# Kernel optimization log

Measured on AMD Instinct MI355X. Metric: run time of the kernel, lower is better.

## Reference

```python
import jax, jax.numpy as jnp
import numpy as np

B, N, M, U, L = 2048, 256, 128, 512, 2   # batch, memory locations, memory width, num_units, num_layers
RH, WH, SH = 2, 2, 1                      # read heads, write heads, conv_shift_range
CLIP = 20.0
HEAD_R = M + 3 + (2 * SH + 1)             # 134 = k(M)+beta+g+s(2r+1)+gamma
HEAD_W = HEAD_R + 2 * M                   # 390 = + erase(M) + add(M)


def setup_inputs():
    key = jax.random.key(0)
    ks = jax.random.split(key, 12)
    def nrm(k, shape, s=0.05):
        return jax.random.normal(k, shape, jnp.float32) * s
    return {
        "X": jax.random.normal(ks[0], (B, U), jnp.float32),
        "m0": nrm(ks[1], (1, N, M), 0.5),
        "H0": nrm(ks[2], (L, 1, U)),
        "C0": nrm(ks[3], (L, 1, U)),
        "R0": nrm(ks[4], (RH, 1, M)),
        "A0": nrm(ks[5], (RH + WH, 1, N)),
        "W_prep": nrm(ks[6], (M * RH, U)),
        "b_prep": jnp.zeros((U,), jnp.float32),
        "W_lstm": nrm(ks[7], (L, 3 * U, 4 * U)),
        "b_lstm": jnp.zeros((L, 4 * U), jnp.float32),
        "W_r": nrm(ks[8], (U, RH * HEAD_R)),
        "b_r": jnp.zeros((RH * HEAD_R,), jnp.float32),
        "W_w": nrm(ks[9], (U, WH * HEAD_W)),
        "b_w": jnp.zeros((WH * HEAD_W,), jnp.float32),
        "W_ou": nrm(ks[10], (U + RH * M, U)),
        "b_ou": jnp.zeros((U,), jnp.float32),
    }


def _addressing(k, beta, g, s, gamma, m, a_prev):
    # k [B,M], beta/g/gamma [B], s [B,2*SH+1], m [B,N,M], a_prev [B,N]
    inner = jnp.einsum('bnm,bm->bn', m, k)
    k_norm = jnp.sqrt(jnp.sum(k * k, axis=1, keepdims=True))   # [B,1]
    m_norm = jnp.sqrt(jnp.sum(m * m, axis=2))                  # [B,N]
    K = inner / (k_norm * m_norm + 1e-8)
    w_c = jax.nn.softmax(beta[:, None] * K, axis=1)            # exp/sum in source == softmax
    w_g = g[:, None] * w_c + (1.0 - g[:, None]) * a_prev
    # The stacked-slice s_matrix in the source is exactly circular convolution:
    # w_conv[i] = sum_d s_d * w_g[(i - d) mod N], d in {0..SH, -SH..-1} matching s layout.
    shifts = list(range(0, SH + 1)) + list(range(-SH, 0))
    w_conv = sum(s[:, j:j + 1] * jnp.roll(w_g, shifts[j], axis=1) for j in range(2 * SH + 1))
    w_sharp = w_conv ** gamma[:, None]
    return w_sharp / jnp.sum(w_sharp, axis=1, keepdims=True)


def reference(X, m0, H0, C0, R0, A0, W_prep, b_prep, W_lstm, b_lstm,
              W_r, b_r, W_w, b_w, W_ou, b_ou):
    b = X.shape[0]
    m = jnp.broadcast_to(m0, (b, N, M))
    R_prev = [jnp.broadcast_to(jnp.tanh(R0[i]), (b, M)) for i in range(RH)]
    A_prev = [jnp.broadcast_to(jax.nn.softmax(A0[i], axis=-1), (b, N)) for i in range(RH + WH)]

    # controller
    h = jnp.concatenate(R_prev, axis=1) @ W_prep + b_prep
    for l in range(L):
        x_in = jnp.concatenate([X, h], axis=1)                              # [B,2U]
        h_prev = jnp.broadcast_to(H0[l], (b, U))
        c_prev = jnp.broadcast_to(C0[l], (b, U))
        z = jnp.concatenate([x_in, h_prev], axis=1) @ W_lstm[l] + b_lstm[l]  # [B,4U]
        i_g, f_g, g_g, o_g = jnp.split(z, 4, axis=1)
        c = jax.nn.sigmoid(f_g) * c_prev + jax.nn.sigmoid(i_g) * jnp.tanh(g_g)
        h = jax.nn.sigmoid(o_g) * jnp.tanh(c)
    h = jnp.clip(h, -CLIP, CLIP)

    r_heads = (h @ W_r + b_r).reshape(b, RH, HEAD_R)
    w_heads = (h @ W_w + b_w).reshape(b, WH, HEAD_W)
    heads = [r_heads[:, i] for i in range(RH)] + [w_heads[:, i] for i in range(WH)]

    A_t = []
    for ii, hd in enumerate(heads):
        A_t.append(_addressing(
            k=jnp.tanh(hd[:, :M]),
            beta=jax.nn.softplus(hd[:, M]),
            g=jax.nn.sigmoid(hd[:, M + 1]),
            s=jax.nn.softmax(hd[:, M + 2:M + 2 + 2 * SH + 1], axis=-1),
            gamma=jax.nn.softplus(hd[:, M + 2 + 2 * SH + 1]),
            m=m, a_prev=A_prev[ii]))

    # reads from old memory
    R_t = [jnp.einsum('bn,bnm->bm', A_t[i], m) for i in range(RH)]

    # sequential erase/add writes
    m_t = m
    for ii in range(WH):
        w = A_t[RH + ii][:, :, None]                                  # [B,N,1]
        del_v = jax.nn.sigmoid(w_heads[:, ii, -2 * M:-M])[:, None, :]  # [B,1,M]
        add_v = jnp.tanh(w_heads[:, ii, -M:])[:, None, :]
        m_t = m_t * (1.0 - w * del_v) + w * add_v

    y = jnp.clip(jnp.concatenate([h] + R_t, axis=1) @ W_ou + b_ou, -CLIP, CLIP)
    return y, m_t
```

## Files before the change

kernel.cpp:

```cpp
#include <hip/hip_runtime.h>
#include <math.h>

static constexpr int Bn = 2048;
static constexpr int Nn = 256;
static constexpr int Mn = 128;
static constexpr int Un = 512;

static constexpr size_t OFF_MNORM = 4608;
static constexpr size_t OFF_APREV = 4864;
static constexpr size_t OFF_BIASH = 5888;
static constexpr size_t OFF_KMAT  = 16384;
static constexpr size_t OFF_HEADS = OFF_KMAT + (size_t)8192 * 256;
static constexpr size_t OFF_AT    = OFF_HEADS + (size_t)2048 * 1048;
static constexpr size_t OFF_ERA   = OFF_AT + (size_t)2 * 2048 * 256;
static constexpr size_t OFF_ADD   = OFF_ERA + (size_t)2048 * 256;
static constexpr size_t OFF_XHB   = OFF_ADD + (size_t)2048 * 256;
static constexpr size_t OFF_HCAT  = OFF_XHB + 524288;
static constexpr size_t OFF_W0T   = OFF_HCAT + 524288;
static constexpr size_t OFF_W1T   = OFF_W0T + 524288;
static constexpr size_t OFF_WRWT  = OFF_W1T + 1048576;
static constexpr size_t OFF_WCOMB = OFF_WRWT + 294912;
static constexpr size_t OFF_WR2T  = OFF_WCOMB + 262144;
static constexpr size_t OFF_M0B   = OFF_WR2T + 65536;
static constexpr size_t OFF_ZPART = OFF_M0B + 16384 + 524288;

static constexpr int P_X0  = 0;
static constexpr int P_M0  = 512;
static constexpr int P_W0  = 528;
static constexpr int P_WR2 = 1552;
static constexpr int P_CA  = 1680;
static constexpr int P_ZC  = 1681;
static constexpr int P_END = 1745;

static constexpr int M_L0  = 0;
static constexpr int M_PF  = 512;
static constexpr int M_W1  = 544;
static constexpr int M_WRr = 2592;
static constexpr int M_WRw = 2736;
static constexpr int M_WOU = 3136;
static constexpr int M_ZC1 = 3392;
static constexpr int M_END = 3456;

static constexpr int T_OUT = 0;
static constexpr int T_MEM = 128;
static constexpr int T_END = 384;

#define DEV __device__ __forceinline__

typedef __attribute__((ext_vector_type(8))) short bf16x8;
typedef __attribute__((ext_vector_type(4))) float f32x4;
typedef __attribute__((ext_vector_type(8))) unsigned short ushort8;
typedef unsigned int u32;

DEV float sigf(float x) { return 1.0f / (1.0f + expf(-x)); }
DEV float softplusf(float x) { return x > 20.0f ? x : log1pf(expf(x)); }
DEV unsigned short f2bf(float f) {
    unsigned u = __float_as_uint(f);
    u = (u + 0x7FFFu + ((u >> 16) & 1u)) >> 16;
    return (unsigned short)u;
}
DEV void gload16(const unsigned short* g, unsigned short* l) {
    __builtin_amdgcn_global_load_lds(
        (const __attribute__((address_space(1))) u32*)g,
        (__attribute__((address_space(3))) u32*)l, 16, 0, 0);
}

DEV float blk_reduce_max(float v, float* red) {
    int tid = threadIdx.x;
    red[tid] = v; __syncthreads();
    for (int s = (int)blockDim.x >> 1; s > 0; s >>= 1) {
        if (tid < s) red[tid] = fmaxf(red[tid], red[tid + s]);
        __syncthreads();
    }
    float r = red[0]; __syncthreads();
    return r;
}
DEV float blk_reduce_sum(float v, float* red) {
    int tid = threadIdx.x;
    red[tid] = v; __syncthreads();
    for (int s = (int)blockDim.x >> 1; s > 0; s >>= 1) {
        if (tid < s) red[tid] += red[tid + s];
        __syncthreads();
    }
    float r = red[0]; __syncthreads();
    return r;
}

DEV float wv_sum(float v) {
    #pragma unroll
    for (int off = 32; off; off >>= 1) v += __shfl_xor(v, off);
    return v;
}
DEV float wv_max(float v) {
    #pragma unroll
    for (int off = 32; off; off >>= 1) v = fmaxf(v, __shfl_xor(v, off));
    return v;
}
DEV float blk_sum4(float v, float* red4) {
    v = wv_sum(v);
    int w = threadIdx.x >> 6;
    if ((threadIdx.x & 63) == 0) red4[w] = v;
    __syncthreads();
    float r = red4[0] + red4[1] + red4[2] + red4[3];
    __syncthreads();
    return r;
}
DEV float blk_max4(float v, float* red4) {
    v = wv_max(v);
    int w = threadIdx.x >> 6;
    if ((threadIdx.x & 63) == 0) red4[w] = v;
    __syncthreads();
    float r = fmaxf(fmaxf(red4[0], red4[1]), fmaxf(red4[2], red4[3]));
    __syncthreads();
    return r;
}

#define GEMM_SHARED                                                             \
    __shared__ __align__(16) unsigned short As[2][64 * 64];                     \
    __shared__ __align__(16) unsigned short Ws[2][128 * 64];

#define GEMM_REGS                                                               \
    const int tid  = threadIdx.x;                                               \
    const int lane = tid & 63;                                                  \
    const int wave = tid >> 6;                                                  \
    const int wr = wave >> 1, wc = wave & 1;                                    \
    const int ke = ((tid & 7) * 8) ^ (((tid >> 3) & 7) << 3);                   \
    const int frow = lane & 15;                                                 \
    const int fko  = (lane >> 4) * 8;                                           \
    const int fxm  = (frow & 7) << 3;                                           \
    f32x4 acc[2][4];                                                            \
    _Pragma("unroll")                                                           \
    for (int i = 0; i < 2; ++i)                                                 \
        _Pragma("unroll")                                                       \
        for (int j = 0; j < 4; ++j) acc[i][j] = (f32x4){0.f, 0.f, 0.f, 0.f};

#define GEMM_STAGE(buf, k0)                                                     \
    {                                                                           \
        _Pragma("unroll")                                                       \
        for (int q = 0; q < 2; ++q)                                             \
            gload16(A  + (size_t)(row0 + q * 32 + (tid >> 3)) * lda + (k0) + ke,\
                    &As[buf][q * 2048 + tid * 8]);                              \
        _Pragma("unroll")                                                       \
        for (int q = 0; q < 4; ++q)                                             \
            gload16(Wt + (size_t)(col0 + q * 32 + (tid >> 3)) * ldw + (k0) + ke,\
                    &Ws[buf][q * 2048 + tid * 8]);                              \
    }

#define GEMM_FRAGS_AND_MFMA(Ab, Wb)                                             \
    {                                                                           \
        bf16x8 af[2][2], wf[2][4];                                              \
        _Pragma("unroll")                                                       \
        for (int kk = 0; kk < 2; ++kk) {                                        \
            _Pragma("unroll")                                                   \
            for (int i = 0; i < 2; ++i) {                                       \
                int fr = wr * 32 + i * 16 + frow;                               \
                af[kk][i] = *(const bf16x8*)&(Ab)[fr * 64 + ((kk * 32 + fko) ^ fxm)]; \
            }                                                                   \
            _Pragma("unroll")                                                   \
            for (int j = 0; j < 4; ++j) {                                       \
                int fr = wc * 64 + j * 16 + frow;                               \
                wf[kk][j] = *(const bf16x8*)&(Wb)[fr * 64 + ((kk * 32 + fko) ^ fxm)]; \
            }                                                                   \
        }                                                                       \
        __builtin_amdgcn_s_setprio(1);                                          \
        _Pragma("unroll")                                                       \
        for (int kk = 0; kk < 2; ++kk)                                          \
            _Pragma("unroll")                                                   \
            for (int i = 0; i < 2; ++i)                                         \
                _Pragma("unroll")                                               \
                for (int j = 0; j < 4; ++j)                                     \
                    acc[i][j] = __builtin_amdgcn_mfma_f32_16x16x32_bf16(        \
                        af[kk][i], wf[kk][j], acc[i][j], 0, 0, 0);              \
        __builtin_amdgcn_s_setprio(0);                                          \
    }

#define GEMM_MAINLOOP(Kr)                                                       \
    {                                                                           \
        const int nt = (Kr) >> 6;                                               \
        int cur = 0;                                                            \
        GEMM_STAGE(0, 0);                                                       \
        for (int t = 0; t < nt; ++t) {                                          \
            if (t + 1 < nt) {                                                   \
                GEMM_STAGE(cur ^ 1, (t + 1) * 64);                              \
                asm volatile("s_waitcnt vmcnt(6)" ::: "memory");                \
            } else {                                                            \
                asm volatile("s_waitcnt vmcnt(0)" ::: "memory");                \
            }                                                                   \
            __builtin_amdgcn_sched_barrier(0);                                  \
            __builtin_amdgcn_s_barrier();                                       \
            __builtin_amdgcn_sched_barrier(0);                                  \
            GEMM_FRAGS_AND_MFMA(As[cur], Ws[cur]);                              \
            __builtin_amdgcn_sched_barrier(0);                                  \
            __builtin_amdgcn_s_barrier();                                       \
            cur ^= 1;                                                           \
        }                                                                       \
    }

#define LSTM_EPILOGUE(zc, doclip, houtp, ldhv)                                  \
    {                                                                           \
        const int uu = lane & 15;                                               \
        const int q  = (col0 >> 6) + wc;                                        \
        const int uq = q * 16 + uu;                                             \
        const float c0v = c0[(zc) * 512 + uq];                                  \
        float bg[4];                                                            \
        _Pragma("unroll")                                                       \
        for (int g = 0; g < 4; ++g) {                                           \
            int j = g * 512 + q * 16 + uu;                                      \
            float a = b_lstm[(zc) * 2048 + j];                                  \
            _Pragma("unroll")                                                   \
            for (int p = 0; p < 8; ++p)                                         \
                a += zpart[((size_t)(zc) * 8 + p) * 2048 + j];                  \
            bg[g] = a;                                                          \
        }                                                                       \
        _Pragma("unroll")                                                       \
        for (int i = 0; i < 2; ++i) {                                           \
            int rbase = row0 + wr * 32 + i * 16 + (lane >> 4) * 4;              \
            _Pragma("unroll")                                                   \
            for (int r = 0; r < 4; ++r) {                                       \
                float ig = acc[i][0][r] + bg[0];                                \
                float fg = acc[i][1][r] + bg[1];                                \
                float gg = acc[i][2][r] + bg[2];                                \
                float og = acc[i][3][r] + bg[3];                                \
                float c = sigf(fg) * c0v + sigf(ig) * tanhf(gg);                \
                float h = sigf(og) * tanhf(c);                                  \
                if (doclip) h = fminf(fmaxf(h, -20.f), 20.f);                   \
                (houtp)[(size_t)(rbase + r) * (ldhv) + uq] = f2bf(h);           \
            }                                                                   \
        }                                                                       \
    }

DEV void dev_cvt8(const float* src, int lds, unsigned short* dst, int ldd,
                  int c8, int bloc, int tid)
{
    size_t idx = (size_t)bloc * 256 + tid;
    size_t r = idx / c8, c = (idx % c8) * 8;
    const float* s = src + r * lds + c;
    float4 v0 = *(const float4*)s;
    float4 v1 = *(const float4*)(s + 4);
    ushort8 o;
    o[0] = f2bf(v0.x); o[1] = f2bf(v0.y); o[2] = f2bf(v0.z); o[3] = f2bf(v0.w);
    o[4] = f2bf(v1.x); o[5] = f2bf(v1.y); o[6] = f2bf(v1.z); o[7] = f2bf(v1.w);
    *(ushort8*)(dst + r * ldd + c) = o;
}

DEV void dev_cvtT(const float* src, int R, int C, int lds,
                  unsigned short* dst, int ldd, int mode, int bx, int by,
                  int tid, float* t )
{
    const int x = tid & 31;
    for (int y = tid >> 5; y < 32; y += 8) {
        int r = by * 32 + y, c = bx * 32 + x;
        int scol = c;
        if (mode) scol = ((c >> 4) & 3) * 512 + (c >> 6) * 16 + (c & 15);
        t[y * 33 + x] = (r < R && c < C) ? src[(size_t)r * lds + scol] : 0.f;
    }
    __syncthreads();
    for (int y = tid >> 5; y < 32; y += 8) {
        int c = bx * 32 + y, r = by * 32 + x;
        if (c < C && r < R) dst[(size_t)c * ldd + r] = f2bf(t[x * 33 + y]);
    }
}

__global__ __launch_bounds__(256) void k_prep(
    const float* __restrict__ X, const float* __restrict__ m0,
    const float* __restrict__ H0, const float* __restrict__ R0,
    const float* __restrict__ A0, const float* __restrict__ W_prep,
    const float* __restrict__ b_prep, const float* __restrict__ W_lstm,
    const float* __restrict__ b_r, const float* __restrict__ b_w,
    const float* __restrict__ W_ou, float* __restrict__ ws)
{
    __shared__ float sh[32 * 33 + 64];
    const int bid = blockIdx.x, tid = threadIdx.x;
    unsigned short* XHB  = (unsigned short*)(ws + OFF_XHB);
    unsigned short* W0T  = (unsigned short*)(ws + OFF_W0T);
    unsigned short* WR2T = (unsigned short*)(ws + OFF_WR2T);
    unsigned short* M0B  = (unsigned short*)(ws + OFF_M0B);

    if (bid < P_M0) {
        dev_cvt8(X, 512, XHB, 1024, 64, bid - P_X0, tid);
    } else if (bid < P_W0) {
        dev_cvt8(m0, 128, M0B, 128, 16, bid - P_M0, tid);
    } else if (bid < P_WR2) {
        int s = bid - P_W0;
        dev_cvtT(W_lstm, 512, 2048, 2048, W0T, 512, 1, s & 63, s >> 6, tid, sh);
    } else if (bid < P_CA) {
        int s = bid - P_WR2;
        dev_cvtT(W_ou + (size_t)512 * 512, 256, 512, 512, WR2T, 256, 0,
                 s & 15, s >> 4, tid, sh);
    } else if (bid < P_ZC) {
        float* red = sh;
        for (int i = 0; i < 4; ++i) {
            float v = A0[i * 256 + tid];
            float mx = blk_reduce_max(v, red);
            float e = expf(v - mx);
            float s = blk_reduce_sum(e, red);
            ws[OFF_APREV + i * 256 + tid] = e / s;
        }
        float acc = 0.f;
        for (int m = 0; m < 128; ++m) {
            float t = m0[(size_t)tid * 128 + m];
            acc = fmaf(t, t, acc);
        }
        ws[OFF_MNORM + tid] = sqrtf(acc);
        for (int j = tid; j < 1152; j += 256)
            ws[OFF_BIASH + j] = (j < 268) ? b_r[j] : (j < 1048 ? b_w[j - 268] : 0.f);
    } else {
        int sub = bid - P_ZC;
        int colb = sub & 7, up = sub >> 3;
        int j = colb * 256 + tid;
        float acc = 0.f;
        if (up < 4) {
            sh[256 + tid] = tanhf(R0[tid]);
            __syncthreads();
            if (tid < 128) {
                int u = up * 128 + tid;
                float a = b_prep[u];
                for (int k = 0; k < 256; ++k)
                    a = fmaf(sh[256 + k], W_prep[(size_t)k * 512 + u], a);
                sh[tid] = a;
            }
            __syncthreads();
            const int u0 = up * 128;
            #pragma unroll 4
            for (int t = 0; t < 128; ++t)
                acc = fmaf(sh[t], W_lstm[(size_t)(512 + u0 + t) * 2048 + j], acc);
        } else {
            const int u0 = up * 128;
            #pragma unroll 4
            for (int t = 0; t < 128; ++t)
                acc = fmaf(H0[u0 - 512 + t],
                           W_lstm[(size_t)(512 + u0 + t) * 2048 + j], acc);
        }
        (ws + OFF_ZPART)[(size_t)up * 2048 + j] = acc;
    }
}

__global__ __launch_bounds__(256) void k_mid(
    const float* __restrict__ W_lstm, const float* __restrict__ W_r,
    const float* __restrict__ W_w, const float* __restrict__ W_ou,
    const float* __restrict__ H0, const float* __restrict__ b_lstm,
    const float* __restrict__ c0, float* __restrict__ ws)
{
    GEMM_SHARED
    const int s = blockIdx.x;
    float* sh = (float*)&As[0][0];
    unsigned short* XHB   = (unsigned short*)(ws + OFF_XHB);
    unsigned short* W0T   = (unsigned short*)(ws + OFF_W0T);
    unsigned short* W1T   = (unsigned short*)(ws + OFF_W1T);
    unsigned short* WRWT  = (unsigned short*)(ws + OFF_WRWT);
    unsigned short* WCOMB = (unsigned short*)(ws + OFF_WCOMB);
    unsigned short* WR2T  = (unsigned short*)(ws + OFF_WR2T);
    unsigned short* M0B   = (unsigned short*)(ws + OFF_M0B);
    const float* zpart    = ws + OFF_ZPART;

    if (s < M_W1) {
        const unsigned short *A, *Wt;
        int lda, ldw, row0, col0, Kr;
        unsigned short* pCb = nullptr;
        const bool lstm0 = (s < M_PF);
        if (lstm0) {
            A = XHB;  lda = 1024; Wt = W0T; ldw = 512;
            row0 = (s & 31) * 64; col0 = (s >> 5) * 128; Kr = 512;
        } else {
            int p = s - M_PF;
            int pz = p >> 4, py = (p >> 3) & 1, px = p & 7;
            A = WR2T + pz * 128; lda = 256; Wt = M0B; ldw = 128;
            row0 = px * 64; col0 = py * 128; Kr = 128;
            pCb = WCOMB + 512 + pz * 256;
        }
        GEMM_REGS
        GEMM_MAINLOOP(Kr)
        if (lstm0) {
            unsigned short* hout = XHB + 512;
            LSTM_EPILOGUE(0, 0, hout, 1024)
        } else {
            #pragma unroll
            for (int i = 0; i < 2; ++i) {
                int m0r = row0 + wr * 32 + i * 16 + (lane >> 4) * 4;
                #pragma unroll
                for (int j = 0; j < 4; ++j) {
                    int n = col0 + wc * 64 + j * 16 + (lane & 15);
                    #pragma unroll
                    for (int r = 0; r < 4; ++r)
                        pCb[(size_t)(m0r + r) * 1024 + n] = f2bf(acc[i][j][r]);
                }
            }
        }
    } else if (s < M_WRr) {
        int s1 = s - M_W1;
        dev_cvtT(W_lstm + (size_t)1536 * 2048, 1024, 2048, 2048, W1T, 1024, 1,
                 s1 & 63, s1 >> 6, threadIdx.x, sh);
    } else if (s < M_WRw) {
        int s2 = s - M_WRr;
        dev_cvtT(W_r, 512, 268, 268, WRWT, 512, 0, s2 % 9, s2 / 9, threadIdx.x, sh);
    } else if (s < M_WOU) {
        int s3 = s - M_WRw;
        dev_cvtT(W_w, 512, 780, 780, WRWT + (size_t)268 * 512, 512, 0,
                 s3 % 25, s3 / 25, threadIdx.x, sh);
    } else if (s < M_ZC1) {
        int s4 = s - M_WOU;
        dev_cvtT(W_ou, 512, 512, 512, WCOMB, 1024, 0, s4 & 15, s4 >> 4,
                 threadIdx.x, sh);
    } else {
        int s5 = s - M_ZC1;
        int colb = s5 & 7, up = s5 >> 3;
        int j = colb * 256 + threadIdx.x;
        const int u0 = up * 64;
        const float* W1 = W_lstm + (size_t)1536 * 2048;
        float acc = 0.f;
        #pragma unroll 4
        for (int t = 0; t < 64; ++t)
            acc = fmaf(H0[512 + u0 + t], W1[(size_t)(1024 + u0 + t) * 2048 + j], acc);
        (ws + OFF_ZPART)[((size_t)8 + up) * 2048 + j] = acc;
    }
}

__global__ __launch_bounds__(256) void gemm_lstm(
    const unsigned short* __restrict__ A, int lda,
    const unsigned short* __restrict__ Wt, int ldw,
    const float* __restrict__ zpart, const float* __restrict__ b_lstm,
    const float* __restrict__ c0, unsigned short* __restrict__ hout)
{
    GEMM_SHARED
    const int row0 = blockIdx.x * 64;
    const int col0 = blockIdx.y * 128;
    GEMM_REGS
    GEMM_MAINLOOP(1024)
    LSTM_EPILOGUE(1, 1, hout, 1024)
}

__global__ __launch_bounds__(256) void gemm_bf16(
    const unsigned short* __restrict__ A, int lda,
    const unsigned short* __restrict__ Wt, int ldw,
    const float* __restrict__ bias, float* __restrict__ C, int ldc,
    int Nr, int Kr)
{
    GEMM_SHARED
    const int row0 = blockIdx.x * 64;
    const int col0 = blockIdx.y * 128;
    GEMM_REGS
    GEMM_MAINLOOP(Kr)
    #pragma unroll
    for (int i = 0; i < 2; ++i) {
        int m0r = row0 + wr * 32 + i * 16 + (lane >> 4) * 4;
        #pragma unroll
        for (int j = 0; j < 4; ++j) {
            int n = col0 + wc * 64 + j * 16 + (lane & 15);
            if (n >= Nr) continue;
            float bv = bias ? bias[n] : 0.f;
            #pragma unroll
            for (int r = 0; r < 4; ++r)
                C[(size_t)(m0r + r) * ldc + n] = acc[i][j][r] + bv;
        }
    }
}

__global__ __launch_bounds__(256) void gemm_kmat(
    const float* __restrict__ heads,
    const unsigned short* __restrict__ M0B,
    float* __restrict__ C)
{
    GEMM_SHARED
    const int row0 = blockIdx.x * 64;
    const int col0 = blockIdx.y * 128;
    GEMM_REGS

#define KMAT_STAGE(buf, k0)                                                     \
    {                                                                           \
        _Pragma("unroll")                                                       \
        for (int q = 0; q < 2; ++q) {                                           \
            int R = row0 + q * 32 + (tid >> 3);                                 \
            int b = R >> 2, ih = R & 3;                                         \
            int cb = (ih < 2) ? ih * 134 : 268 + (ih - 2) * 390;                \
            const float* hp = heads + (size_t)b * 1048 + cb + (k0) + ke;        \
            ushort8 o;                                                          \
            _Pragma("unroll")                                                   \
            for (int j = 0; j < 8; ++j) o[j] = f2bf(tanhf(hp[j]));              \
            *(ushort8*)&As[buf][q * 2048 + tid * 8] = o;                        \
        }                                                                       \
        _Pragma("unroll")                                                       \
        for (int q = 0; q < 4; ++q)                                             \
            gload16(M0B + (size_t)(col0 + q * 32 + (tid >> 3)) * 128 + (k0) + ke,\
                    &Ws[buf][q * 2048 + tid * 8]);                              \
    }

    int cur = 0;
    KMAT_STAGE(0, 0);
    for (int t = 0; t < 2; ++t) {
        __syncthreads();
        if (t == 0) KMAT_STAGE(1, 64);
        GEMM_FRAGS_AND_MFMA(As[cur], Ws[cur]);
        cur ^= 1;
    }
#undef KMAT_STAGE
    #pragma unroll
    for (int i = 0; i < 2; ++i) {
        int m0r = row0 + wr * 32 + i * 16 + (lane >> 4) * 4;
        #pragma unroll
        for (int j = 0; j < 4; ++j) {
            int n = col0 + wc * 64 + j * 16 + (lane & 15);
            #pragma unroll
            for (int r = 0; r < 4; ++r)
                C[(size_t)(m0r + r) * 256 + n] = acc[i][j][r];
        }
    }
}

__global__ __launch_bounds__(256) void k_addr(
    const float* __restrict__ heads, const float* __restrict__ kmat,
    const float* __restrict__ mnorm, const float* __restrict__ aprev,
    float* __restrict__ at, unsigned short* __restrict__ hcat,
    float* __restrict__ era, float* __restrict__ addv)
{
    __shared__ float red4[4];
    __shared__ float wgs[256];
    __shared__ float sc[6];
    const int b = blockIdx.x, i = blockIdx.y, tid = threadIdx.x;
    const int cb = (i < 2) ? i * 134 : 268 + (i - 2) * 390;
    const float* hd = heads + (size_t)b * 1048 + cb;
    float kv = (tid < 128) ? tanhf(hd[tid]) : 0.f;
    float kn = sqrtf(blk_sum4(kv * kv, red4));
    if (i >= 2 && tid < 128) {
        era [((size_t)b * 2 + (i - 2)) * 128 + tid] = sigf(hd[134 + tid]);
        addv[((size_t)b * 2 + (i - 2)) * 128 + tid] = tanhf(hd[262 + tid]);
    }
    if (tid == 0) {
        sc[0] = softplusf(hd[128]);
        sc[1] = sigf(hd[129]);
        float v0 = hd[130], v1 = hd[131], v2 = hd[132];
        float mx = fmaxf(v0, fmaxf(v1, v2));
        float e0 = expf(v0 - mx), e1 = expf(v1 - mx), e2 = expf(v2 - mx);
        float ssum = e0 + e1 + e2;
        sc[2] = e0 / ssum; sc[3] = e1 / ssum; sc[4] = e2 / ssum;
        sc[5] = softplusf(hd[133]);
    }
    __syncthreads();
    const float beta = sc[0], g = sc[1], s0 = sc[2], s1 = sc[3], s2 = sc[4],
                gamma = sc[5];
    float inner = kmat[((size_t)b * 4 + i) * 256 + tid];
    float K = inner / (kn * mnorm[tid] + 1e-8f);
    float x = beta * K;
    float mx = blk_max4(x, red4);
    float e = expf(x - mx);
    float se = blk_sum4(e, red4);
    float wc = e / se;
    float wg = g * wc + (1.f - g) * aprev[i * 256 + tid];
    wgs[tid] = wg;
    __syncthreads();
    float wconv = s0 * wg + s1 * wgs[(tid + 255) & 255] + s2 * wgs[(tid + 1) & 255];
    float wsh = powf(wconv, gamma);
    float ssum = blk_sum4(wsh, red4);
    float w = wsh / ssum;
    if (i < 2) hcat[(size_t)b * 1024 + 512 + i * 256 + tid] = f2bf(w);
    else       at[((size_t)(i - 2) * Bn + b) * 256 + tid] = w;
}

__global__ __launch_bounds__(256) void k_tail(
    const unsigned short* __restrict__ HCAT,
    const unsigned short* __restrict__ WCOMB,
    const float* __restrict__ b_ou,
    const float* __restrict__ m0, const float* __restrict__ at,
    const float* __restrict__ era, const float* __restrict__ addv,
    float* __restrict__ out)
{
    GEMM_SHARED
    const int s = blockIdx.x;
    if (s < T_MEM) {
        const unsigned short* A  = HCAT;  const int lda = 1024;
        const unsigned short* Wt = WCOMB; const int ldw = 1024;
        const int row0 = (s & 31) * 64;
        const int col0 = (s >> 5) * 128;
        GEMM_REGS
        GEMM_MAINLOOP(1024)
        #pragma unroll
        for (int i = 0; i < 2; ++i) {
            int m0r = row0 + wr * 32 + i * 16 + (lane >> 4) * 4;
            #pragma unroll
            for (int j = 0; j < 4; ++j) {
                int n = col0 + wc * 64 + j * 16 + (lane & 15);
                if (n >= 512) continue;
                float bv = b_ou[n];
                #pragma unroll
                for (int r = 0; r < 4; ++r) {
                    float v = acc[i][j][r] + bv;
                    out[(size_t)(m0r + r) * 512 + n] = fminf(fmaxf(v, -20.f), 20.f);
                }
            }
        }
    } else {
        const int tid = threadIdx.x;
        const int b0 = (s - T_MEM) * 8;
        float (*at_s)[8][256] = (float(*)[8][256])(&As[0][0]);
        float (*er_s)[8][128] = (float(*)[8][128])(&Ws[0][0]);
        float (*ad_s)[8][128] = (float(*)[8][128])(&Ws[0][4096]);
        for (int t = tid; t < 1024; t += 256) {
            int i = t >> 9, rem = t & 511;
            int bb = rem >> 6, n4 = rem & 63;
            ((float4*)&at_s[i][bb][0])[n4] =
                ((const float4*)(at + ((size_t)i * Bn + b0 + bb) * 256))[n4];
        }
        for (int t = tid; t < 512; t += 256) {
            int i = t >> 8, rem = t & 255;
            int bb = rem >> 5, m4 = rem & 31;
            ((float4*)&er_s[i][bb][0])[m4] =
                ((const float4*)(era + ((size_t)(b0 + bb) * 2 + i) * 128))[m4];
            ((float4*)&ad_s[i][bb][0])[m4] =
                ((const float4*)(addv + ((size_t)(b0 + bb) * 2 + i) * 128))[m4];
        }
        __syncthreads();
        const float4* m0v = (const float4*)m0;
        float4* outv = (float4*)(out + (size_t)Bn * Un);
        for (int pos = tid; pos < 8192; pos += 256) {
            int mq = pos & 31, n = pos >> 5;
            float4 t0 = m0v[pos];
            #pragma unroll
            for (int bb = 0; bb < 8; ++bb) {
                float w0 = at_s[0][bb][n], w1 = at_s[1][bb][n];
                float4 e0 = *(const float4*)&er_s[0][bb][mq * 4];
                float4 a0 = *(const float4*)&ad_s[0][bb][mq * 4];
                float4 e1 = *(const float4*)&er_s[1][bb][mq * 4];
                float4 a1 = *(const float4*)&ad_s[1][bb][mq * 4];
                float4 t = t0;
#define UPD(c) { t.c = t.c * (1.f - w0 * e0.c) + w0 * a0.c; \
                 t.c = t.c * (1.f - w1 * e1.c) + w1 * a1.c; }
                UPD(x) UPD(y) UPD(z) UPD(w)
#undef UPD
                __builtin_nontemporal_store(*(f32x4*)&t,
                    (f32x4*)&outv[(size_t)(b0 + bb) * 8192 + pos]);
            }
        }
    }
}

extern "C" void kernel_launch(void* const* d_in, const int* in_sizes, int n_in,
                              void* d_out, int out_size, void* d_ws, size_t ws_size,
                              hipStream_t stream)
{
    const float* X      = (const float*)d_in[0];
    const float* m0     = (const float*)d_in[1];
    const float* H0     = (const float*)d_in[2];
    const float* C0     = (const float*)d_in[3];
    const float* R0     = (const float*)d_in[4];
    const float* A0     = (const float*)d_in[5];
    const float* W_prep = (const float*)d_in[6];
    const float* b_prep = (const float*)d_in[7];
    const float* W_lstm = (const float*)d_in[8];
    const float* b_lstm = (const float*)d_in[9];
    const float* W_r    = (const float*)d_in[10];
    const float* b_r    = (const float*)d_in[11];
    const float* W_w    = (const float*)d_in[12];
    const float* b_w    = (const float*)d_in[13];
    const float* W_ou   = (const float*)d_in[14];
    const float* b_ou   = (const float*)d_in[15];
    float* ws  = (float*)d_ws;
    float* out = (float*)d_out;

    unsigned short* XHB   = (unsigned short*)(ws + OFF_XHB);
    unsigned short* HCAT  = (unsigned short*)(ws + OFF_HCAT);
    unsigned short* W1T   = (unsigned short*)(ws + OFF_W1T);
    unsigned short* WRWT  = (unsigned short*)(ws + OFF_WRWT);
    unsigned short* WCOMB = (unsigned short*)(ws + OFF_WCOMB);
    unsigned short* M0B   = (unsigned short*)(ws + OFF_M0B);

    k_prep<<<P_END, 256, 0, stream>>>(
        X, m0, H0, R0, A0, W_prep, b_prep, W_lstm, b_r, b_w, W_ou, ws);

    k_mid<<<M_END, 256, 0, stream>>>(
        W_lstm, W_r, W_w, W_ou, H0, b_lstm, C0, ws);

    gemm_lstm<<<dim3(32, 16), 256, 0, stream>>>(
        XHB, 1024, W1T, 1024, ws + OFF_ZPART, b_lstm, C0, HCAT);

    gemm_bf16<<<dim3(32, 9), 256, 0, stream>>>(
        HCAT, 1024, WRWT, 512, ws + OFF_BIASH, ws + OFF_HEADS, 1048, 1048, 512);

    gemm_kmat<<<dim3(128, 2), 256, 0, stream>>>(
        ws + OFF_HEADS, M0B, ws + OFF_KMAT);

    k_addr<<<dim3(Bn, 4), 256, 0, stream>>>(
        ws + OFF_HEADS, ws + OFF_KMAT, ws + OFF_MNORM, ws + OFF_APREV,
        ws + OFF_AT, HCAT, ws + OFF_ERA, ws + OFF_ADD);

    k_tail<<<T_END, 256, 0, stream>>>(
        HCAT, WCOMB, b_ou, m0, ws + OFF_AT, ws + OFF_ERA, ws + OFF_ADD, out);
}
```

Before: 175.7 us.

## Split LSTM layer-1 and output GEMMs to move independent halves earlier

The layer-1 LSTM GEMM is split. The X-dependent half (x times W1 input rows) is now computed in k_mid alongside layer 0 and stored as bf16 in the KMAT scratch region, so gemm_lstm runs only K=512 over the h0 half and adds the stored partial in its epilogue. Likewise, the h-part of the output projection is computed in the new k_heads kernel next to the head GEMM, which leaves k_tail with only the read-vector half. The W1 transpose moves into k_prep. The intent is to shorten the serial critical path and fill more CUs per launch, at the cost of extra bf16/fp32 intermediate traffic and bf16 rounding of the partial sum.

```diff
diff --git a/kernel.cpp b/kernel.cpp
--- a/kernel.cpp
+++ b/kernel.cpp
@@ -10,36 +10,42 @@
 static constexpr size_t OFF_APREV = 4864;
 static constexpr size_t OFF_BIASH = 5888;
 static constexpr size_t OFF_KMAT  = 16384;
-static constexpr size_t OFF_HEADS = OFF_KMAT + (size_t)8192 * 256;
-static constexpr size_t OFF_AT    = OFF_HEADS + (size_t)2048 * 1048;
-static constexpr size_t OFF_ERA   = OFF_AT + (size_t)2 * 2048 * 256;
-static constexpr size_t OFF_ADD   = OFF_ERA + (size_t)2048 * 256;
-static constexpr size_t OFF_XHB   = OFF_ADD + (size_t)2048 * 256;
-static constexpr size_t OFF_HCAT  = OFF_XHB + 524288;
-static constexpr size_t OFF_W0T   = OFF_HCAT + 524288;
+static constexpr size_t OFF_HEADS = OFF_KMAT + 2097152;
+static constexpr size_t OFF_AT    = OFF_HEADS + 2146304;
+static constexpr size_t OFF_ERA   = OFF_AT + 1048576;
+static constexpr size_t OFF_ADD   = OFF_ERA + 524288;
+static constexpr size_t OFF_XHB   = OFF_ADD + 524288;
+static constexpr size_t OFF_HCAT  = OFF_XHB + 1048576;
+static constexpr size_t OFF_W0T   = OFF_HCAT + 1048576;
 static constexpr size_t OFF_W1T   = OFF_W0T + 524288;
 static constexpr size_t OFF_WRWT  = OFF_W1T + 1048576;
 static constexpr size_t OFF_WCOMB = OFF_WRWT + 294912;
 static constexpr size_t OFF_WR2T  = OFF_WCOMB + 262144;
 static constexpr size_t OFF_M0B   = OFF_WR2T + 65536;
-static constexpr size_t OFF_ZPART = OFF_M0B + 16384 + 524288;
+static constexpr size_t OFF_ZPART = OFF_M0B + 16384;
+static constexpr size_t OFF_YH    = OFF_ZPART + 32768;
 
 static constexpr int P_X0  = 0;
 static constexpr int P_M0  = 512;
 static constexpr int P_W0  = 528;
-static constexpr int P_WR2 = 1552;
-static constexpr int P_CA  = 1680;
-static constexpr int P_ZC  = 1681;
-static constexpr int P_END = 1745;
+static constexpr int P_W1  = 1552;
+static constexpr int P_WR2 = 3600;
+static constexpr int P_CA  = 3728;
+static constexpr int P_ZC  = 3729;
+static constexpr int P_END = 3793;
 
 static constexpr int M_L0  = 0;
-static constexpr int M_PF  = 512;
-static constexpr int M_W1  = 544;
-static constexpr int M_WRr = 2592;
-static constexpr int M_WRw = 2736;
-static constexpr int M_WOU = 3136;
-static constexpr int M_ZC1 = 3392;
-static constexpr int M_END = 3456;
+static constexpr int M_ZX  = 512;
+static constexpr int M_PF  = 1024;
+static constexpr int M_WRr = 1056;
+static constexpr int M_WRw = 1200;
+static constexpr int M_WOU = 1600;
+static constexpr int M_ZC1 = 1856;
+static constexpr int M_END = 1920;
+
+static constexpr int H_HD  = 0;
+static constexpr int H_YH  = 288;
+static constexpr int H_END = 416;
 
 static constexpr int T_OUT = 0;
 static constexpr int T_MEM = 128;
@@ -59,6 +65,7 @@
     u = (u + 0x7FFFu + ((u >> 16) & 1u)) >> 16;
     return (unsigned short)u;
 }
+DEV float b2f(unsigned short u) { return __uint_as_float((u32)u << 16); }
 DEV void gload16(const unsigned short* g, unsigned short* l) {
     __builtin_amdgcn_global_load_lds(
         (const __attribute__((address_space(1))) u32*)g,
@@ -196,7 +203,7 @@
         }                                                                       \
     }
 
-#define LSTM_EPILOGUE(zc, doclip, houtp, ldhv)                                  \
+#define LSTM_EPILOGUE(zc, doclip, houtp, ldhv, ZXP)                             \
     {                                                                           \
         const int uu = lane & 15;                                               \
         const int q  = (col0 >> 6) + wc;                                        \
@@ -217,10 +224,17 @@
             int rbase = row0 + wr * 32 + i * 16 + (lane >> 4) * 4;              \
             _Pragma("unroll")                                                   \
             for (int r = 0; r < 4; ++r) {                                       \
-                float ig = acc[i][0][r] + bg[0];                                \
-                float fg = acc[i][1][r] + bg[1];                                \
-                float gg = acc[i][2][r] + bg[2];                                \
-                float og = acc[i][3][r] + bg[3];                                \
+                float z0 = 0.f, z1 = 0.f, z2 = 0.f, z3 = 0.f;                   \
+                if (ZXP) {                                                      \
+                    const unsigned short* zr = (ZXP) +                          \
+                        (size_t)(rbase + r) * 2048 + q * 64 + uu;               \
+                    z0 = b2f(zr[0]);  z1 = b2f(zr[16]);                         \
+                    z2 = b2f(zr[32]); z3 = b2f(zr[48]);                         \
+                }                                                               \
+                float ig = acc[i][0][r] + bg[0] + z0;                           \
+                float fg = acc[i][1][r] + bg[1] + z1;                           \
+                float gg = acc[i][2][r] + bg[2] + z2;                           \
+                float og = acc[i][3][r] + bg[3] + z3;                           \
                 float c = sigf(fg) * c0v + sigf(ig) * tanhf(gg);                \
                 float h = sigf(og) * tanhf(c);                                  \
                 if (doclip) h = fminf(fmaxf(h, -20.f), 20.f);                   \
@@ -273,6 +287,7 @@
     const int bid = blockIdx.x, tid = threadIdx.x;
     unsigned short* XHB  = (unsigned short*)(ws + OFF_XHB);
     unsigned short* W0T  = (unsigned short*)(ws + OFF_W0T);
+    unsigned short* W1T  = (unsigned short*)(ws + OFF_W1T);
     unsigned short* WR2T = (unsigned short*)(ws + OFF_WR2T);
     unsigned short* M0B  = (unsigned short*)(ws + OFF_M0B);
 
@@ -280,9 +295,13 @@
         dev_cvt8(X, 512, XHB, 1024, 64, bid - P_X0, tid);
     } else if (bid < P_W0) {
         dev_cvt8(m0, 128, M0B, 128, 16, bid - P_M0, tid);
-    } else if (bid < P_WR2) {
+    } else if (bid < P_W1) {
         int s = bid - P_W0;
         dev_cvtT(W_lstm, 512, 2048, 2048, W0T, 512, 1, s & 63, s >> 6, tid, sh);
+    } else if (bid < P_WR2) {
+        int s = bid - P_W1;
+        dev_cvtT(W_lstm + (size_t)1536 * 2048, 1024, 2048, 2048, W1T, 1024, 1,
+                 s & 63, s >> 6, tid, sh);
     } else if (bid < P_CA) {
         int s = bid - P_WR2;
         dev_cvtT(W_ou + (size_t)512 * 512, 256, 512, 512, WR2T, 256, 0,
@@ -351,18 +370,25 @@
     unsigned short* WCOMB = (unsigned short*)(ws + OFF_WCOMB);
     unsigned short* WR2T  = (unsigned short*)(ws + OFF_WR2T);
     unsigned short* M0B   = (unsigned short*)(ws + OFF_M0B);
+    unsigned short* ZX    = (unsigned short*)(ws + OFF_KMAT);
     const float* zpart    = ws + OFF_ZPART;
 
-    if (s < M_W1) {
+    if (s < M_WRr) {
         const unsigned short *A, *Wt;
-        int lda, ldw, row0, col0, Kr;
+        int lda, ldw, row0, col0, Kr, mode;
         unsigned short* pCb = nullptr;
-        const bool lstm0 = (s < M_PF);
-        if (lstm0) {
+        if (s < M_ZX) {
+            mode = 0;
             A = XHB;  lda = 1024; Wt = W0T; ldw = 512;
             row0 = (s & 31) * 64; col0 = (s >> 5) * 128; Kr = 512;
+        } else if (s < M_PF) {
+            int p = s - M_ZX;
+            mode = 1;
+            A = XHB;  lda = 1024; Wt = W1T; ldw = 1024;
+            row0 = (p & 31) * 64; col0 = (p >> 5) * 128; Kr = 512;
         } else {
             int p = s - M_PF;
+            mode = 2;
             int pz = p >> 4, py = (p >> 3) & 1, px = p & 7;
             A = WR2T + pz * 128; lda = 256; Wt = M0B; ldw = 128;
             row0 = px * 64; col0 = py * 128; Kr = 128;
@@ -370,9 +396,22 @@
         }
         GEMM_REGS
         GEMM_MAINLOOP(Kr)
-        if (lstm0) {
+        if (mode == 0) {
             unsigned short* hout = XHB + 512;
-            LSTM_EPILOGUE(0, 0, hout, 1024)
+            const unsigned short* zxn = nullptr;
+            LSTM_EPILOGUE(0, 0, hout, 1024, zxn)
+        } else if (mode == 1) {
+            #pragma unroll
+            for (int i = 0; i < 2; ++i) {
+                int m0r = row0 + wr * 32 + i * 16 + (lane >> 4) * 4;
+                #pragma unroll
+                for (int j = 0; j < 4; ++j) {
+                    int n = col0 + wc * 64 + j * 16 + (lane & 15);
+                    #pragma unroll
+                    for (int r = 0; r < 4; ++r)
+                        ZX[(size_t)(m0r + r) * 2048 + n] = f2bf(acc[i][j][r]);
+                }
+            }
         } else {
             #pragma unroll
             for (int i = 0; i < 2; ++i) {
@@ -386,10 +425,6 @@
                 }
             }
         }
-    } else if (s < M_WRr) {
-        int s1 = s - M_W1;
-        dev_cvtT(W_lstm + (size_t)1536 * 2048, 1024, 2048, 2048, W1T, 1024, 1,
-                 s1 & 63, s1 >> 6, threadIdx.x, sh);
     } else if (s < M_WRw) {
         int s2 = s - M_WRr;
         dev_cvtT(W_r, 512, 268, 268, WRWT, 512, 0, s2 % 9, s2 / 9, threadIdx.x, sh);
@@ -419,38 +454,64 @@
     const unsigned short* __restrict__ A, int lda,
     const unsigned short* __restrict__ Wt, int ldw,
     const float* __restrict__ zpart, const float* __restrict__ b_lstm,
-    const float* __restrict__ c0, unsigned short* __restrict__ hout)
+    const float* __restrict__ c0, const unsigned short* __restrict__ ZXP,
+    unsigned short* __restrict__ hout)
 {
     GEMM_SHARED
     const int row0 = blockIdx.x * 64;
     const int col0 = blockIdx.y * 128;
     GEMM_REGS
-    GEMM_MAINLOOP(1024)
-    LSTM_EPILOGUE(1, 1, hout, 1024)
-}
-
-__global__ __launch_bounds__(256) void gemm_bf16(
-    const unsigned short* __restrict__ A, int lda,
-    const unsigned short* __restrict__ Wt, int ldw,
-    const float* __restrict__ bias, float* __restrict__ C, int ldc,
-    int Nr, int Kr)
+    GEMM_MAINLOOP(512)
+    LSTM_EPILOGUE(1, 1, hout, 1024, ZXP)
+}
+
+__global__ __launch_bounds__(256) void k_heads(
+    const unsigned short* __restrict__ HCAT,
+    const unsigned short* __restrict__ WRWT,
+    const unsigned short* __restrict__ WCOMB,
+    const float* __restrict__ biash,
+    float* __restrict__ heads, float* __restrict__ yh)
 {
     GEMM_SHARED
-    const int row0 = blockIdx.x * 64;
-    const int col0 = blockIdx.y * 128;
+    const int s = blockIdx.x;
+    const unsigned short* A = HCAT;  const int lda = 1024;
+    const unsigned short* Wt;
+    int ldw, row0, col0;
+    if (s < H_YH) {
+        Wt = WRWT; ldw = 512;
+        row0 = (s & 31) * 64; col0 = (s >> 5) * 128;
+    } else {
+        int p = s - H_YH;
+        Wt = WCOMB; ldw = 1024;
+        row0 = (p & 31) * 64; col0 = (p >> 5) * 128;
+    }
     GEMM_REGS
-    GEMM_MAINLOOP(Kr)
-    #pragma unroll
-    for (int i = 0; i < 2; ++i) {
-        int m0r = row0 + wr * 32 + i * 16 + (lane >> 4) * 4;
+    GEMM_MAINLOOP(512)
+    if (s < H_YH) {
         #pragma unroll
-        for (int j = 0; j < 4; ++j) {
-            int n = col0 + wc * 64 + j * 16 + (lane & 15);
-            if (n >= Nr) continue;
-            float bv = bias ? bias[n] : 0.f;
+        for (int i = 0; i < 2; ++i) {
+            int m0r = row0 + wr * 32 + i * 16 + (lane >> 4) * 4;
             #pragma unroll
-            for (int r = 0; r < 4; ++r)
-                C[(size_t)(m0r + r) * ldc + n] = acc[i][j][r] + bv;
+            for (int j = 0; j < 4; ++j) {
+                int n = col0 + wc * 64 + j * 16 + (lane & 15);
+                if (n >= 1048) continue;
+                float bv = biash[n];
+                #pragma unroll
+                for (int r = 0; r < 4; ++r)
+                    heads[(size_t)(m0r + r) * 1048 + n] = acc[i][j][r] + bv;
+            }
+        }
+    } else {
+        #pragma unroll
+        for (int i = 0; i < 2; ++i) {
+            int m0r = row0 + wr * 32 + i * 16 + (lane >> 4) * 4;
+            #pragma unroll
+            for (int j = 0; j < 4; ++j) {
+                int n = col0 + wc * 64 + j * 16 + (lane & 15);
+                #pragma unroll
+                for (int r = 0; r < 4; ++r)
+                    yh[(size_t)(m0r + r) * 512 + n] = acc[i][j][r];
+            }
         }
     }
 }
@@ -558,7 +619,7 @@
 __global__ __launch_bounds__(256) void k_tail(
     const unsigned short* __restrict__ HCAT,
     const unsigned short* __restrict__ WCOMB,
-    const float* __restrict__ b_ou,
+    const float* __restrict__ yh, const float* __restrict__ b_ou,
     const float* __restrict__ m0, const float* __restrict__ at,
     const float* __restrict__ era, const float* __restrict__ addv,
     float* __restrict__ out)
@@ -566,12 +627,12 @@
     GEMM_SHARED
     const int s = blockIdx.x;
     if (s < T_MEM) {
-        const unsigned short* A  = HCAT;  const int lda = 1024;
-        const unsigned short* Wt = WCOMB; const int ldw = 1024;
+        const unsigned short* A  = HCAT + 512;        const int lda = 1024;
+        const unsigned short* Wt = WCOMB + 512;       const int ldw = 1024;
         const int row0 = (s & 31) * 64;
         const int col0 = (s >> 5) * 128;
         GEMM_REGS
-        GEMM_MAINLOOP(1024)
+        GEMM_MAINLOOP(512)
         #pragma unroll
         for (int i = 0; i < 2; ++i) {
             int m0r = row0 + wr * 32 + i * 16 + (lane >> 4) * 4;
@@ -582,7 +643,7 @@
                 float bv = b_ou[n];
                 #pragma unroll
                 for (int r = 0; r < 4; ++r) {
-                    float v = acc[i][j][r] + bv;
+                    float v = acc[i][j][r] + bv + yh[(size_t)(m0r + r) * 512 + n];
                     out[(size_t)(m0r + r) * 512 + n] = fminf(fmaxf(v, -20.f), 20.f);
                 }
             }
@@ -661,6 +722,7 @@
     unsigned short* WRWT  = (unsigned short*)(ws + OFF_WRWT);
     unsigned short* WCOMB = (unsigned short*)(ws + OFF_WCOMB);
     unsigned short* M0B   = (unsigned short*)(ws + OFF_M0B);
+    unsigned short* ZX    = (unsigned short*)(ws + OFF_KMAT);
 
     k_prep<<<P_END, 256, 0, stream>>>(
         X, m0, H0, R0, A0, W_prep, b_prep, W_lstm, b_r, b_w, W_ou, ws);
@@ -669,10 +731,10 @@
         W_lstm, W_r, W_w, W_ou, H0, b_lstm, C0, ws);
 
     gemm_lstm<<<dim3(32, 16), 256, 0, stream>>>(
-        XHB, 1024, W1T, 1024, ws + OFF_ZPART, b_lstm, C0, HCAT);
-
-    gemm_bf16<<<dim3(32, 9), 256, 0, stream>>>(
-        HCAT, 1024, WRWT, 512, ws + OFF_BIASH, ws + OFF_HEADS, 1048, 1048, 512);
+        XHB + 512, 1024, W1T + 512, 1024, ws + OFF_ZPART, b_lstm, C0, ZX, HCAT);
+
+    k_heads<<<H_END, 256, 0, stream>>>(
+        HCAT, WRWT, WCOMB, ws + OFF_BIASH, ws + OFF_HEADS, ws + OFF_YH);
 
     gemm_kmat<<<dim3(128, 2), 256, 0, stream>>>(
         ws + OFF_HEADS, M0B, ws + OFF_KMAT);
@@ -682,5 +744,6 @@
         ws + OFF_AT, HCAT, ws + OFF_ERA, ws + OFF_ADD);
 
     k_tail<<<T_END, 256, 0, stream>>>(
-        HCAT, WCOMB, b_ou, m0, ws + OFF_AT, ws + OFF_ERA, ws + OFF_ADD, out);
-}
+        HCAT, WCOMB, ws + OFF_YH, b_ou, m0, ws + OFF_AT, ws + OFF_ERA,
+        ws + OFF_ADD, out);
+}
```

New measurement: 173.5 us, median of 2. No clear change (-1.3%).
